# Kernel tuning notes

Hardware: AMD Instinct MI355X
Metric: run time of the kernel (lower is better)

Reference implementation:

```python
import jax, jax.numpy as jnp
import numpy as np

EMB = 1024
HEADS = 16
HEAD_DIM = EMB // HEADS


def setup_inputs() -> dict:
    key = jax.random.key(0)
    ks = jax.random.split(key, 5)
    scale = 1.0 / np.sqrt(EMB)
    x = jax.random.normal(ks[0], (4, 2048, EMB), dtype=jnp.float32)
    w_qkv = jax.random.uniform(ks[1], (3 * EMB, EMB), jnp.float32, -scale, scale)
    b_qkv = jax.random.uniform(ks[2], (3 * EMB,), jnp.float32, -scale, scale)
    w_proj = jax.random.uniform(ks[3], (EMB, EMB), jnp.float32, -scale, scale)
    b_proj = jax.random.uniform(ks[4], (EMB,), jnp.float32, -scale, scale)
    return {"x": x, "w_qkv": w_qkv, "b_qkv": b_qkv, "w_proj": w_proj, "b_proj": b_proj}


def reference(x, w_qkv, b_qkv, w_proj, b_proj):
    b, n, _ = x.shape
    # qkv: [b, n, 3*emb] -> [3, b, h, n, d]
    qkv = x @ w_qkv.T + b_qkv
    qkv = qkv.reshape(b, n, 3, HEADS, HEAD_DIM).transpose(2, 0, 3, 1, 4)
    q, k, v = qkv[0], qkv[1], qkv[2]
    energy = jnp.einsum('bhqd,bhkd->bhqk', q, k) / np.sqrt(HEAD_DIM).astype(np.float32)
    att = jax.nn.softmax(energy, axis=-1)
    out = jnp.einsum('bhqk,bhkd->bhqd', att, v)
    out = out.transpose(0, 2, 1, 3).reshape(b, n, EMB)
    return out @ w_proj.T + b_proj
```

## Files before the change

kernel.cpp:

```cpp
#include <hip/hip_runtime.h>
#include <math.h>

#define B_    4
#define NS    2048
#define EMB_  1024
#define NH    16
#define HD    64
#define MR    (B_*NS)

typedef __attribute__((ext_vector_type(8))) short bf16x8;
typedef __attribute__((ext_vector_type(4))) float f32x4;

#define AS1 __attribute__((address_space(1)))
#define AS3 __attribute__((address_space(3)))

#if __has_builtin(__builtin_amdgcn_exp2f)
#define EXP2F(x) __builtin_amdgcn_exp2f(x)
#else
#define EXP2F(x) exp2f(x)
#endif

__device__ __forceinline__ unsigned short f2bf(float f) {
  unsigned int x = __float_as_uint(f);
  x += 0x7fffu + ((x >> 16) & 1u);
  return (unsigned short)(x >> 16);
}

__device__ __forceinline__ unsigned int cvt_pk_bf16(float lo, float hi) {
  unsigned int r;
  asm("v_cvt_pk_bf16_f32 %0, %1, %2" : "=v"(r) : "v"(lo), "v"(hi));
  return r;
}

__global__ __launch_bounds__(256) void cvt_kernel(
    const float* __restrict__ x,  unsigned short* __restrict__ xb,  int nx,
    const float* __restrict__ w1, unsigned short* __restrict__ w1b, int n1,
    const float* __restrict__ w2, unsigned short* __restrict__ w2b, int n2) {
  const int total = (nx + n1 + n2) >> 2;
  for (int i = blockIdx.x * blockDim.x + threadIdx.x; i < total;
       i += gridDim.x * blockDim.x) {
    const int idx = i << 2;
    const float* src;
    unsigned short* dst;
    if (idx < nx)            { src = x  + idx;            dst = xb  + idx; }
    else if (idx < nx + n1)  { src = w1 + (idx - nx);     dst = w1b + (idx - nx); }
    else                     { src = w2 + (idx - nx - n1); dst = w2b + (idx - nx - n1); }
    float4 v = *reinterpret_cast<const float4*>(src);
    uint2 p;
    p.x = (unsigned)f2bf(v.x) | ((unsigned)f2bf(v.y) << 16);
    p.y = (unsigned)f2bf(v.z) | ((unsigned)f2bf(v.w) << 16);
    *reinterpret_cast<uint2*>(dst) = p;
  }
}

__device__ __forceinline__ void mfma_mainloop(
    const unsigned short* __restrict__ xg,
    const unsigned short* __restrict__ wg,
    unsigned short* Xs, unsigned short* Ws, f32x4 acc[4][4]) {
  const int tid = threadIdx.x;
  const int w = tid >> 6, l = tid & 63;
  const int lr = l & 15, lq = l >> 4;
  const int wm = w >> 1, wn = w & 1;
  const int rr = l >> 3;
  const int sl = (l & 7) ^ rr;

  for (int kt = 0; kt < 16; ++kt) {
    const int k0 = kt * 64;
#pragma unroll
    for (int i = 0; i < 4; ++i) {
      const int r0 = w * 32 + i * 8;
      __builtin_amdgcn_global_load_lds(
          (const AS1 unsigned int*)(const void*)(xg + (size_t)(r0 + rr) * 1024 + k0 + sl * 8),
          (AS3 unsigned int*)(void*)(Xs + r0 * 64), 16, 0, 0);
      __builtin_amdgcn_global_load_lds(
          (const AS1 unsigned int*)(const void*)(wg + (size_t)(r0 + rr) * 1024 + k0 + sl * 8),
          (AS3 unsigned int*)(void*)(Ws + r0 * 64), 16, 0, 0);
    }
    __syncthreads();

#pragma unroll
    for (int ks = 0; ks < 2; ++ks) {
      bf16x8 xf[4], wf[4];
#pragma unroll
      for (int i = 0; i < 4; ++i) {
        const int row = wm * 64 + i * 16 + lr;
        const int s2 = (ks * 4 + lq) ^ (row & 7);
        xf[i] = *reinterpret_cast<const bf16x8*>((const char*)Xs + row * 128 + s2 * 16);
      }
#pragma unroll
      for (int j = 0; j < 4; ++j) {
        const int row = wn * 64 + j * 16 + lr;
        const int s2 = (ks * 4 + lq) ^ (row & 7);
        wf[j] = *reinterpret_cast<const bf16x8*>((const char*)Ws + row * 128 + s2 * 16);
      }
#pragma unroll
      for (int i = 0; i < 4; ++i)
#pragma unroll
        for (int j = 0; j < 4; ++j)
          acc[i][j] = __builtin_amdgcn_mfma_f32_16x16x32_bf16(wf[j], xf[i], acc[i][j], 0, 0, 0);
    }
    __syncthreads();
  }
}

__global__ __launch_bounds__(256) void qkv_mfma_kernel(
    const unsigned short* __restrict__ xb, const unsigned short* __restrict__ wqb,
    const float* __restrict__ bias,
    unsigned short* __restrict__ qb, unsigned short* __restrict__ kb,
    unsigned short* __restrict__ vtb) {
  __shared__ __align__(16) unsigned short Xs[128 * 64];
  __shared__ __align__(16) unsigned short Ws[128 * 64];
  f32x4 acc[4][4];
  const f32x4 fz = {0.f, 0.f, 0.f, 0.f};
#pragma unroll
  for (int i = 0; i < 4; ++i)
#pragma unroll
    for (int j = 0; j < 4; ++j) acc[i][j] = fz;

  const int bm = blockIdx.x * 128, bn = blockIdx.y * 128;
  mfma_mainloop(xb + (size_t)bm * 1024, wqb + (size_t)bn * 1024, Xs, Ws, acc);

  const int tid = threadIdx.x;
  const int w = tid >> 6, l = tid & 63;
  const int lr = l & 15, lq = l >> 4;
  const int wm = w >> 1, wn = w & 1;
#pragma unroll
  for (int i = 0; i < 4; ++i) {
    const int mrow = bm + wm * 64 + i * 16 + lr;
    const int b = mrow >> 11;
    const int nseq = mrow & (NS - 1);
#pragma unroll
    for (int j = 0; j < 4; ++j) {
      const int col0 = bn + wn * 64 + j * 16 + lq * 4;
      const int which = col0 >> 10;
      const int e = col0 & 1023;
      const int hh = e >> 6, d0 = e & 63;
      const float v0 = acc[i][j][0] + bias[col0 + 0];
      const float v1 = acc[i][j][1] + bias[col0 + 1];
      const float v2 = acc[i][j][2] + bias[col0 + 2];
      const float v3 = acc[i][j][3] + bias[col0 + 3];
      if (which < 2) {
        unsigned short* dst = (which == 0) ? qb : kb;
        const float sc = (which == 0) ? 0.18033688f : 1.0f;
        uint2 pk;
        pk.x = (unsigned)f2bf(v0 * sc) | ((unsigned)f2bf(v1 * sc) << 16);
        pk.y = (unsigned)f2bf(v2 * sc) | ((unsigned)f2bf(v3 * sc) << 16);
        *reinterpret_cast<uint2*>(&dst[(((size_t)b * NH + hh) * NS + nseq) * HD + d0]) = pk;
      } else {
        unsigned short* dt =
            vtb + (((size_t)b * NH + hh) * HD + d0) * NS + nseq;
        dt[0 * NS] = f2bf(v0);
        dt[1 * NS] = f2bf(v1);
        dt[2 * NS] = f2bf(v2);
        dt[3 * NS] = f2bf(v3);
      }
    }
  }
}

__global__ __launch_bounds__(256) void proj_mfma_kernel(
    const unsigned short* __restrict__ attb, const unsigned short* __restrict__ wpb,
    const float* __restrict__ bias, float* __restrict__ out) {
  __shared__ __align__(16) unsigned short Xs[128 * 64];
  __shared__ __align__(16) unsigned short Ws[128 * 64];
  f32x4 acc[4][4];
  const f32x4 fz = {0.f, 0.f, 0.f, 0.f};
#pragma unroll
  for (int i = 0; i < 4; ++i)
#pragma unroll
    for (int j = 0; j < 4; ++j) acc[i][j] = fz;

  const int bm = blockIdx.x * 128, bn = blockIdx.y * 128;
  mfma_mainloop(attb + (size_t)bm * 1024, wpb + (size_t)bn * 1024, Xs, Ws, acc);

  const int tid = threadIdx.x;
  const int w = tid >> 6, l = tid & 63;
  const int lr = l & 15, lq = l >> 4;
  const int wm = w >> 1, wn = w & 1;
#pragma unroll
  for (int i = 0; i < 4; ++i) {
    const int mrow = bm + wm * 64 + i * 16 + lr;
#pragma unroll
    for (int j = 0; j < 4; ++j) {
      const int col0 = bn + wn * 64 + j * 16 + lq * 4;
      const float4 b4 = *reinterpret_cast<const float4*>(&bias[col0]);
      float4 v;
      v.x = acc[i][j][0] + b4.x; v.y = acc[i][j][1] + b4.y;
      v.z = acc[i][j][2] + b4.z; v.w = acc[i][j][3] + b4.w;
      *reinterpret_cast<float4*>(&out[(size_t)mrow * EMB_ + col0]) = v;
    }
  }
}

__global__ __launch_bounds__(256) void attn_mfma2_kernel(
    const unsigned short* __restrict__ qb, const unsigned short* __restrict__ kb,
    const unsigned short* __restrict__ vt, unsigned short* __restrict__ attb) {
  __shared__ __align__(16) unsigned short Ks[2][64 * 64];
  __shared__ __align__(16) unsigned short VT[2][64 * 64];
  __shared__ __align__(16) unsigned short Ps[4][16 * 64];

  const int wg = blockIdx.x;
  const int swz = (wg & 7) * 256 + (wg >> 3);
  const int qblk = swz & 31;
  const int head = swz >> 5;
  const int h = head & 15;
  const int bq = head >> 4;
  const int q0 = qblk * 64;

  const int tid = threadIdx.x;
  const int w = tid >> 6, l = tid & 63;
  const int lr = l & 15, lq = l >> 4;
  const size_t headoff = ((size_t)bq * NH + h) * (size_t)NS * HD;
  const unsigned short* qp = qb + headoff;
  const unsigned short* kp = kb + headoff;
  const unsigned short* vtp = vt + headoff;

  bf16x8 qf[2];
  {
    const unsigned short* qrow = qp + (size_t)(q0 + w * 16 + lr) * HD + lq * 8;
    qf[0] = *reinterpret_cast<const bf16x8*>(qrow);
    qf[1] = *reinterpret_cast<const bf16x8*>(qrow + 32);
  }

  const f32x4 fz = {0.f, 0.f, 0.f, 0.f};
  float m_ = -1e30f, l_ = 0.f;
  f32x4 o_[4];
#pragma unroll
  for (int d = 0; d < 4; ++d) o_[d] = fz;

  const int srow = l >> 3, sslot = l & 7;

#pragma unroll
  for (int n = 0; n < 2; ++n) {
    const int r0 = (n * 4 + w) * 8;
    const int row = r0 + srow;
    const int so = (sslot ^ (row & 7)) * 8;
    __builtin_amdgcn_global_load_lds(
        (const AS1 unsigned int*)(const void*)(kp + row * 64 + so),
        (AS3 unsigned int*)(void*)(&Ks[0][0] + r0 * 64), 16, 0, 0);
    __builtin_amdgcn_global_load_lds(
        (const AS1 unsigned int*)(const void*)(vtp + (size_t)row * NS + so),
        (AS3 unsigned int*)(void*)(&VT[0][0] + r0 * 64), 16, 0, 0);
  }
  __syncthreads();

  int buf = 0;
  for (int kt = 0; kt < NS / 64; ++kt) {
    if (kt < NS / 64 - 1) {
      const unsigned short* knext = kp + (size_t)(kt + 1) * 64 * 64;
      const int vcol = (kt + 1) * 64;
#pragma unroll
      for (int n = 0; n < 2; ++n) {
        const int r0 = (n * 4 + w) * 8;
        const int row = r0 + srow;
        const int so = (sslot ^ (row & 7)) * 8;
        __builtin_amdgcn_global_load_lds(
            (const AS1 unsigned int*)(const void*)(knext + row * 64 + so),
            (AS3 unsigned int*)(void*)(&Ks[buf ^ 1][0] + r0 * 64), 16, 0, 0);
        __builtin_amdgcn_global_load_lds(
            (const AS1 unsigned int*)(const void*)(vtp + (size_t)row * NS + vcol + so),
            (AS3 unsigned int*)(void*)(&VT[buf ^ 1][0] + r0 * 64), 16, 0, 0);
      }
    }

    f32x4 s_[4];
#pragma unroll
    for (int j4 = 0; j4 < 4; ++j4) s_[j4] = fz;
#pragma unroll
    for (int ks = 0; ks < 2; ++ks) {
#pragma unroll
      for (int j4 = 0; j4 < 4; ++j4) {
        const int row = j4 * 16 + lr;
        const int s2 = (ks * 4 + lq) ^ (row & 7);
        bf16x8 kf = *reinterpret_cast<const bf16x8*>((const char*)&Ks[buf][0] + row * 128 + s2 * 16);
        s_[j4] = __builtin_amdgcn_mfma_f32_16x16x32_bf16(kf, qf[ks], s_[j4], 0, 0, 0);
      }
    }

    float tm = fmaxf(fmaxf(fmaxf(s_[0][0], s_[0][1]), fmaxf(s_[0][2], s_[0][3])),
                     fmaxf(fmaxf(s_[1][0], s_[1][1]), fmaxf(s_[1][2], s_[1][3])));
    tm = fmaxf(tm, fmaxf(fmaxf(fmaxf(s_[2][0], s_[2][1]), fmaxf(s_[2][2], s_[2][3])),
                         fmaxf(fmaxf(s_[3][0], s_[3][1]), fmaxf(s_[3][2], s_[3][3]))));
    tm = fmaxf(tm, __shfl_xor(tm, 16, 64));
    tm = fmaxf(tm, __shfl_xor(tm, 32, 64));
    if (!__all(tm <= m_ + 11.5416f)) {
      const float nm = fmaxf(m_, tm);
      const float fac = EXP2F(m_ - nm);
      m_ = nm;
      l_ *= fac;
#pragma unroll
      for (int r = 0; r < 4; ++r) {
        const float fr = __shfl(fac, (l & 48) | (lq * 4 + r), 64);
        o_[0][r] *= fr; o_[1][r] *= fr; o_[2][r] *= fr; o_[3][r] *= fr;
      }
    }
    float rs = 0.f;
#pragma unroll
    for (int j4 = 0; j4 < 4; ++j4) {
      const float p0 = EXP2F(s_[j4][0] - m_);
      const float p1 = EXP2F(s_[j4][1] - m_);
      const float p2 = EXP2F(s_[j4][2] - m_);
      const float p3 = EXP2F(s_[j4][3] - m_);
      rs += (p0 + p1) + (p2 + p3);
      const int s16 = (j4 * 2 + (lq >> 1)) ^ (lr & 7);
      uint2 pk;
      pk.x = cvt_pk_bf16(p0, p1);
      pk.y = cvt_pk_bf16(p2, p3);
      *reinterpret_cast<uint2*>((char*)&Ps[w][0] + lr * 128 + s16 * 16 + (lq & 1) * 8) = pk;
    }
    rs += __shfl_xor(rs, 16, 64);
    rs += __shfl_xor(rs, 32, 64);
    l_ += rs;

#pragma unroll
    for (int ks = 0; ks < 2; ++ks) {
      const int sp = (ks * 4 + lq) ^ (lr & 7);
      bf16x8 pf = *reinterpret_cast<const bf16x8*>((const char*)&Ps[w][0] + lr * 128 + sp * 16);
#pragma unroll
      for (int d = 0; d < 4; ++d) {
        const int rowv = d * 16 + lr;
        const int s2 = (ks * 4 + lq) ^ (rowv & 7);
        bf16x8 vf = *reinterpret_cast<const bf16x8*>((const char*)&VT[buf][0] + rowv * 128 + s2 * 16);
        o_[d] = __builtin_amdgcn_mfma_f32_16x16x32_bf16(pf, vf, o_[d], 0, 0, 0);
      }
    }
    __syncthreads();
    buf ^= 1;
  }

#pragma unroll
  for (int r = 0; r < 4; ++r) {
    const float lsum = __shfl(l_, (l & 48) | (lq * 4 + r), 64);
    const float inv = 1.0f / lsum;
    const size_t row = (size_t)bq * NS + q0 + w * 16 + lq * 4 + r;
#pragma unroll
    for (int d = 0; d < 4; ++d) {
      attb[row * EMB_ + h * HD + d * 16 + lr] = f2bf(o_[d][r] * inv);
    }
  }
}

extern "C" void kernel_launch(void* const* d_in, const int* in_sizes, int n_in,
                              void* d_out, int out_size, void* d_ws, size_t ws_size,
                              hipStream_t stream) {
  const float* x      = (const float*)d_in[0];
  const float* w_qkv  = (const float*)d_in[1];
  const float* b_qkv  = (const float*)d_in[2];
  const float* w_proj = (const float*)d_in[3];
  const float* b_proj = (const float*)d_in[4];
  float* out = (float*)d_out;

  const size_t per = (size_t)B_ * NH * NS * HD;
  unsigned short* qb   = (unsigned short*)d_ws;
  unsigned short* kb   = qb + per;
  unsigned short* vtb  = kb + per;
  unsigned short* attb = vtb + per;
  unsigned short* xb   = attb + (size_t)MR * EMB_;
  unsigned short* wqb  = xb + (size_t)MR * EMB_;
  unsigned short* wpb  = wqb + (size_t)3 * EMB_ * EMB_;

  const int nx = MR * EMB_;
  const int n1 = 3 * EMB_ * EMB_;
  const int n2 = EMB_ * EMB_;
  cvt_kernel<<<2048, 256, 0, stream>>>(x, xb, nx, w_qkv, wqb, n1, w_proj, wpb, n2);

  dim3 g1(MR / 128, 3 * EMB_ / 128);
  qkv_mfma_kernel<<<g1, 256, 0, stream>>>(xb, wqb, b_qkv, qb, kb, vtb);

  attn_mfma2_kernel<<<2048, 256, 0, stream>>>(qb, kb, vtb, attb);

  dim3 g3(MR / 128, EMB_ / 128);
  proj_mfma_kernel<<<g3, 256, 0, stream>>>(attb, wpb, b_proj, out);
}
```

Measured before the change: 223.2 us.

## Process two 64-row query sub-blocks per attention workgroup to reuse K/V tiles

Each attention workgroup now handles 128 query rows (two 64-row sub-blocks per wave set) instead of 64, so every K and V tile loaded into LDS is used twice. This halves global K/V traffic and the number of barriers per query row, and the grid shrinks from 2048 to 1024 workgroups. In exchange each thread holds twice the accumulators and softmax state, which raises register pressure, and there are fewer workgroups to spread across the CUs.

```diff
diff --git a/kernel.cpp b/kernel.cpp
--- a/kernel.cpp
+++ b/kernel.cpp
@@ -192,7 +192,7 @@
   }
 }
 
-__global__ __launch_bounds__(256) void attn_mfma2_kernel(
+__global__ __launch_bounds__(256) void attn_mfma7_kernel(
     const unsigned short* __restrict__ qb, const unsigned short* __restrict__ kb,
     const unsigned short* __restrict__ vt, unsigned short* __restrict__ attb) {
   __shared__ __align__(16) unsigned short Ks[2][64 * 64];
@@ -200,12 +200,12 @@
   __shared__ __align__(16) unsigned short Ps[4][16 * 64];
 
   const int wg = blockIdx.x;
-  const int swz = (wg & 7) * 256 + (wg >> 3);
-  const int qblk = swz & 31;
-  const int head = swz >> 5;
+  const int swz = (wg & 7) * 128 + (wg >> 3);
+  const int qblk = swz & 15;
+  const int head = swz >> 4;
   const int h = head & 15;
   const int bq = head >> 4;
-  const int q0 = qblk * 64;
+  const int q0 = qblk * 128;
 
   const int tid = threadIdx.x;
   const int w = tid >> 6, l = tid & 63;
@@ -215,18 +215,22 @@
   const unsigned short* kp = kb + headoff;
   const unsigned short* vtp = vt + headoff;
 
-  bf16x8 qf[2];
-  {
-    const unsigned short* qrow = qp + (size_t)(q0 + w * 16 + lr) * HD + lq * 8;
-    qf[0] = *reinterpret_cast<const bf16x8*>(qrow);
-    qf[1] = *reinterpret_cast<const bf16x8*>(qrow + 32);
+  bf16x8 qf[2][2];
+#pragma unroll
+  for (int qs = 0; qs < 2; ++qs) {
+    const unsigned short* qrow =
+        qp + (size_t)(q0 + qs * 64 + w * 16 + lr) * HD + lq * 8;
+    qf[qs][0] = *reinterpret_cast<const bf16x8*>(qrow);
+    qf[qs][1] = *reinterpret_cast<const bf16x8*>(qrow + 32);
   }
 
   const f32x4 fz = {0.f, 0.f, 0.f, 0.f};
-  float m_ = -1e30f, l_ = 0.f;
-  f32x4 o_[4];
-#pragma unroll
-  for (int d = 0; d < 4; ++d) o_[d] = fz;
+  float m_[2] = {-1e30f, -1e30f}, l_[2] = {0.f, 0.f};
+  f32x4 o_[2][4];
+#pragma unroll
+  for (int qs = 0; qs < 2; ++qs)
+#pragma unroll
+    for (int d = 0; d < 4; ++d) o_[qs][d] = fz;
 
   const int srow = l >> 3, sslot = l & 7;
 
@@ -263,65 +267,69 @@
       }
     }
 
-    f32x4 s_[4];
-#pragma unroll
-    for (int j4 = 0; j4 < 4; ++j4) s_[j4] = fz;
-#pragma unroll
-    for (int ks = 0; ks < 2; ++ks) {
+#pragma unroll
+    for (int qs = 0; qs < 2; ++qs) {
+      f32x4 s_[4];
+#pragma unroll
+      for (int j4 = 0; j4 < 4; ++j4) s_[j4] = fz;
+#pragma unroll
+      for (int ks = 0; ks < 2; ++ks) {
+#pragma unroll
+        for (int j4 = 0; j4 < 4; ++j4) {
+          const int row = j4 * 16 + lr;
+          const int s2 = (ks * 4 + lq) ^ (row & 7);
+          bf16x8 kf = *reinterpret_cast<const bf16x8*>((const char*)&Ks[buf][0] + row * 128 + s2 * 16);
+          s_[j4] = __builtin_amdgcn_mfma_f32_16x16x32_bf16(kf, qf[qs][ks], s_[j4], 0, 0, 0);
+        }
+      }
+
+      float tm = fmaxf(fmaxf(fmaxf(s_[0][0], s_[0][1]), fmaxf(s_[0][2], s_[0][3])),
+                       fmaxf(fmaxf(s_[1][0], s_[1][1]), fmaxf(s_[1][2], s_[1][3])));
+      tm = fmaxf(tm, fmaxf(fmaxf(fmaxf(s_[2][0], s_[2][1]), fmaxf(s_[2][2], s_[2][3])),
+                           fmaxf(fmaxf(s_[3][0], s_[3][1]), fmaxf(s_[3][2], s_[3][3]))));
+      tm = fmaxf(tm, __shfl_xor(tm, 16, 64));
+      tm = fmaxf(tm, __shfl_xor(tm, 32, 64));
+      if (!__all(tm <= m_[qs] + 11.5416f)) {
+        const float nm = fmaxf(m_[qs], tm);
+        const float fac = EXP2F(m_[qs] - nm);
+        m_[qs] = nm;
+        l_[qs] *= fac;
+#pragma unroll
+        for (int r = 0; r < 4; ++r) {
+          const float fr = __shfl(fac, (l & 48) | (lq * 4 + r), 64);
+          o_[qs][0][r] *= fr; o_[qs][1][r] *= fr;
+          o_[qs][2][r] *= fr; o_[qs][3][r] *= fr;
+        }
+      }
+      float rs = 0.f;
 #pragma unroll
       for (int j4 = 0; j4 < 4; ++j4) {
-        const int row = j4 * 16 + lr;
-        const int s2 = (ks * 4 + lq) ^ (row & 7);
-        bf16x8 kf = *reinterpret_cast<const bf16x8*>((const char*)&Ks[buf][0] + row * 128 + s2 * 16);
-        s_[j4] = __builtin_amdgcn_mfma_f32_16x16x32_bf16(kf, qf[ks], s_[j4], 0, 0, 0);
-      }
-    }
-
-    float tm = fmaxf(fmaxf(fmaxf(s_[0][0], s_[0][1]), fmaxf(s_[0][2], s_[0][3])),
-                     fmaxf(fmaxf(s_[1][0], s_[1][1]), fmaxf(s_[1][2], s_[1][3])));
-    tm = fmaxf(tm, fmaxf(fmaxf(fmaxf(s_[2][0], s_[2][1]), fmaxf(s_[2][2], s_[2][3])),
-                         fmaxf(fmaxf(s_[3][0], s_[3][1]), fmaxf(s_[3][2], s_[3][3]))));
-    tm = fmaxf(tm, __shfl_xor(tm, 16, 64));
-    tm = fmaxf(tm, __shfl_xor(tm, 32, 64));
-    if (!__all(tm <= m_ + 11.5416f)) {
-      const float nm = fmaxf(m_, tm);
-      const float fac = EXP2F(m_ - nm);
-      m_ = nm;
-      l_ *= fac;
-#pragma unroll
-      for (int r = 0; r < 4; ++r) {
-        const float fr = __shfl(fac, (l & 48) | (lq * 4 + r), 64);
-        o_[0][r] *= fr; o_[1][r] *= fr; o_[2][r] *= fr; o_[3][r] *= fr;
-      }
-    }
-    float rs = 0.f;
-#pragma unroll
-    for (int j4 = 0; j4 < 4; ++j4) {
-      const float p0 = EXP2F(s_[j4][0] - m_);
-      const float p1 = EXP2F(s_[j4][1] - m_);
-      const float p2 = EXP2F(s_[j4][2] - m_);
-      const float p3 = EXP2F(s_[j4][3] - m_);
-      rs += (p0 + p1) + (p2 + p3);
-      const int s16 = (j4 * 2 + (lq >> 1)) ^ (lr & 7);
-      uint2 pk;
-      pk.x = cvt_pk_bf16(p0, p1);
-      pk.y = cvt_pk_bf16(p2, p3);
-      *reinterpret_cast<uint2*>((char*)&Ps[w][0] + lr * 128 + s16 * 16 + (lq & 1) * 8) = pk;
-    }
-    rs += __shfl_xor(rs, 16, 64);
-    rs += __shfl_xor(rs, 32, 64);
-    l_ += rs;
-
-#pragma unroll
-    for (int ks = 0; ks < 2; ++ks) {
-      const int sp = (ks * 4 + lq) ^ (lr & 7);
-      bf16x8 pf = *reinterpret_cast<const bf16x8*>((const char*)&Ps[w][0] + lr * 128 + sp * 16);
-#pragma unroll
-      for (int d = 0; d < 4; ++d) {
-        const int rowv = d * 16 + lr;
-        const int s2 = (ks * 4 + lq) ^ (rowv & 7);
-        bf16x8 vf = *reinterpret_cast<const bf16x8*>((const char*)&VT[buf][0] + rowv * 128 + s2 * 16);
-        o_[d] = __builtin_amdgcn_mfma_f32_16x16x32_bf16(pf, vf, o_[d], 0, 0, 0);
+        const float p0 = EXP2F(s_[j4][0] - m_[qs]);
+        const float p1 = EXP2F(s_[j4][1] - m_[qs]);
+        const float p2 = EXP2F(s_[j4][2] - m_[qs]);
+        const float p3 = EXP2F(s_[j4][3] - m_[qs]);
+        rs += (p0 + p1) + (p2 + p3);
+        const int s16 = (j4 * 2 + (lq >> 1)) ^ (lr & 7);
+        uint2 pk;
+        pk.x = cvt_pk_bf16(p0, p1);
+        pk.y = cvt_pk_bf16(p2, p3);
+        *reinterpret_cast<uint2*>((char*)&Ps[w][0] + lr * 128 + s16 * 16 + (lq & 1) * 8) = pk;
+      }
+      rs += __shfl_xor(rs, 16, 64);
+      rs += __shfl_xor(rs, 32, 64);
+      l_[qs] += rs;
+
+#pragma unroll
+      for (int ks = 0; ks < 2; ++ks) {
+        const int sp = (ks * 4 + lq) ^ (lr & 7);
+        bf16x8 pf = *reinterpret_cast<const bf16x8*>((const char*)&Ps[w][0] + lr * 128 + sp * 16);
+#pragma unroll
+        for (int d = 0; d < 4; ++d) {
+          const int rowv = d * 16 + lr;
+          const int s2 = (ks * 4 + lq) ^ (rowv & 7);
+          bf16x8 vf = *reinterpret_cast<const bf16x8*>((const char*)&VT[buf][0] + rowv * 128 + s2 * 16);
+          o_[qs][d] = __builtin_amdgcn_mfma_f32_16x16x32_bf16(pf, vf, o_[qs][d], 0, 0, 0);
+        }
       }
     }
     __syncthreads();
@@ -329,15 +337,17 @@
   }
 
 #pragma unroll
-  for (int r = 0; r < 4; ++r) {
-    const float lsum = __shfl(l_, (l & 48) | (lq * 4 + r), 64);
-    const float inv = 1.0f / lsum;
-    const size_t row = (size_t)bq * NS + q0 + w * 16 + lq * 4 + r;
-#pragma unroll
-    for (int d = 0; d < 4; ++d) {
-      attb[row * EMB_ + h * HD + d * 16 + lr] = f2bf(o_[d][r] * inv);
-    }
-  }
+  for (int qs = 0; qs < 2; ++qs)
+#pragma unroll
+    for (int r = 0; r < 4; ++r) {
+      const float lsum = __shfl(l_[qs], (l & 48) | (lq * 4 + r), 64);
+      const float inv = 1.0f / lsum;
+      const size_t row = (size_t)bq * NS + q0 + qs * 64 + w * 16 + lq * 4 + r;
+#pragma unroll
+      for (int d = 0; d < 4; ++d) {
+        attb[row * EMB_ + h * HD + d * 16 + lr] = f2bf(o_[qs][d][r] * inv);
+      }
+    }
 }
 
 extern "C" void kernel_launch(void* const* d_in, const int* in_sizes, int n_in,
@@ -367,7 +377,7 @@
   dim3 g1(MR / 128, 3 * EMB_ / 128);
   qkv_mfma_kernel<<<g1, 256, 0, stream>>>(xb, wqb, b_qkv, qb, kb, vtb);
 
-  attn_mfma2_kernel<<<2048, 256, 0, stream>>>(qb, kb, vtb, attb);
+  attn_mfma7_kernel<<<1024, 256, 0, stream>>>(qb, kb, vtb, attb);
 
   dim3 g3(MR / 128, EMB_ / 128);
   proj_mfma_kernel<<<g3, 256, 0, stream>>>(attb, wpb, b_proj, out);
```

Result: no change. 225.3 us (+0.9%).
